# Performance work log

Hardware: AMD Instinct MI355X
Metric: run time of the kernel (lower is better)

## Reference

```python
import jax, jax.numpy as jnp
import numpy as np

N, E, IN_DIM, HID = 50000, 800000, 128, 64
NEG_SLOPE = 0.01  # torch F.leaky_relu default


def setup_inputs() -> dict:
    key = jax.random.key(0)
    ks = jax.random.split(key, 8)
    x = jax.random.normal(ks[0], (N, IN_DIM), jnp.float32)
    edge_index = jax.random.randint(ks[1], (2, E), 0, N, dtype=jnp.int32)
    edge_weight = jax.random.uniform(ks[2], (E,), jnp.float32)
    h = jnp.zeros((N, HID), jnp.float32)
    c = jnp.zeros((N, HID), jnp.float32)
    sx = 1.0 / np.sqrt(IN_DIM)
    sh = 1.0 / np.sqrt(HID)
    # gate order along leading axis: [i, f, c(tilde), o]; K=2 Chebyshev weights
    Wx = (jax.random.normal(ks[3], (4, 2, IN_DIM, HID), jnp.float32) * sx)
    bx = jnp.zeros((4, HID), jnp.float32)
    Wh = (jax.random.normal(ks[4], (4, 2, HID, HID), jnp.float32) * sh)
    bh = jnp.zeros((4, HID), jnp.float32)
    wc = jax.random.normal(ks[5], (3, HID), jnp.float32) * 0.1  # peepholes for i, f, o
    bg = jnp.zeros((4, HID), jnp.float32)
    W_head = jax.random.normal(ks[6], (HID, 1), jnp.float32) * sh
    b_head = jnp.zeros((1,), jnp.float32)
    return dict(x=x, edge_index=edge_index, edge_weight=edge_weight, h=h, c=c,
                Wx=Wx, bx=bx, Wh=Wh, bh=bh, wc=wc, bg=bg, W_head=W_head, b_head=b_head)


def _cheb_norm(src, dst, ew, n):
    # ChebConv 'sym' normalization with lambda_max=2: L_hat = -D^{-1/2} A D^{-1/2}
    # (the +1 self-loop from the Laplacian cancels against fill_value=-1)
    deg = jnp.zeros((n,), ew.dtype).at[src].add(ew)
    dinv = jnp.where(deg > 0, 1.0 / jnp.sqrt(jnp.where(deg > 0, deg, 1.0)), 0.0)
    return -dinv[src] * ew * dinv[dst]


def _prop(feat, src, dst, norm, n):
    # T1 = L_hat @ feat via edge gather + segment-sum
    return jax.ops.segment_sum(norm[:, None] * feat[src], dst, num_segments=n)


def reference(x, edge_index, edge_weight, h, c, Wx, bx, Wh, bh, wc, bg, W_head, b_head):
    n = x.shape[0]
    src, dst = edge_index[0], edge_index[1]
    norm = _cheb_norm(src, dst, edge_weight, n)
    Tx = _prop(x, src, dst, norm, n)
    Th = _prop(h, src, dst, norm, n)  # shared across all 4 h-side ChebConvs
    # z[g] = X W[g,0] + (L_hat X) W[g,1] + b  for all gates at once
    z = (jnp.einsum('nd,gdh->gnh', x, Wx[:, 0]) + jnp.einsum('nd,gdh->gnh', Tx, Wx[:, 1]) + bx[:, None, :]
         + jnp.einsum('nd,gdh->gnh', h, Wh[:, 0]) + jnp.einsum('nd,gdh->gnh', Th, Wh[:, 1]) + bh[:, None, :])
    i = jax.nn.sigmoid(z[0] + wc[0] * c + bg[0])
    f = jax.nn.sigmoid(z[1] + wc[1] * c + bg[1])
    g = jnp.tanh(z[2] + bg[2])
    c_new = f * c + i * g
    o = jax.nn.sigmoid(z[3] + wc[2] * c_new + bg[3])
    h_new = o * jnp.tanh(c_new)
    out = jax.nn.leaky_relu(h_new, NEG_SLOPE) @ W_head + b_head
    return out, h_new, c_new
```

## Files before the change

### kernel.cpp

```cpp
#include <hip/hip_runtime.h>
#include <hip/hip_bf16.h>

#define IN_DIM 128
#define HID 64
#define NEG_SLOPE 0.01f
#define CAP 5120

typedef __attribute__((ext_vector_type(8))) short short8;
typedef __attribute__((ext_vector_type(4))) short short4v;
typedef __attribute__((ext_vector_type(4))) float f32x4;
typedef unsigned short ushort_t;
typedef unsigned int uint_t;

__device__ __forceinline__ float fsig(float x) { return 1.f / (1.f + __expf(-x)); }
__device__ __forceinline__ float ftanh(float x) { return 1.f - 2.f / (__expf(2.f * x) + 1.f); }

__device__ __forceinline__ ushort_t f2bf(float f) {
    uint_t u = __float_as_uint(f);
    uint_t r = u + 0x7fffu + ((u >> 16) & 1u);
    return (ushort_t)(r >> 16);
}
__device__ __forceinline__ float bf2f(ushort_t s) { return __uint_as_float(((uint_t)s) << 16); }
__device__ __forceinline__ float bf2f_s(short s) { return bf2f((ushort_t)s); }

__global__ __launch_bounds__(256) void part_kernel(
    const int* __restrict__ src, const int* __restrict__ dst, const float* __restrict__ ew,
    const float* __restrict__ x, const float* __restrict__ h,
    const float* __restrict__ Wx, const float* __restrict__ Wh,
    int* __restrict__ cur_d, int* __restrict__ cur_s,
    int2* __restrict__ dpart, int2* __restrict__ spart,
    uint_t* __restrict__ xb_u, uint_t* __restrict__ hb_u, ushort_t* __restrict__ Wp,
    int E, int N, int nbPart) {
    __shared__ int hd[256], hs[256];
    int t = threadIdx.x;

    if ((int)blockIdx.x < nbPart) {
        hd[t] = 0; hs[t] = 0;
        __syncthreads();
        int base = blockIdx.x * 2048;
        int sv[8], dv[8]; float wv[8];
#pragma unroll
        for (int it = 0; it < 8; ++it) {
            int e = base + it * 256 + t;
            bool ok = e < E;
            sv[it] = ok ? src[e] : 0;
            dv[it] = ok ? dst[e] : 0;
            wv[it] = ok ? ew[e] : 0.f;
            if (ok) {
                atomicAdd(&hd[dv[it] >> 8], 1);
                atomicAdd(&hs[sv[it] >> 8], 1);
            }
        }
        __syncthreads();
        int nd = hd[t], ns = hs[t];
        __syncthreads();
        if (nd) hd[t] = atomicAdd(&cur_d[t * 16], nd);
        if (ns) hs[t] = atomicAdd(&cur_s[t * 16], ns);
        __syncthreads();
#pragma unroll
        for (int it = 0; it < 8; ++it) {
            int e = base + it * 256 + t;
            if (e < E) {
                int d = dv[it], s = sv[it];
                int bd = d >> 8, bs = s >> 8;
                int pd = atomicAdd(&hd[bd], 1);
                int ps = atomicAdd(&hs[bs], 1);
                dpart[(size_t)bd * CAP + pd] = make_int2(s | ((d & 255) << 16), __float_as_int(wv[it]));
                spart[(size_t)bs * CAP + ps] = make_int2(s & 255, __float_as_int(wv[it]));
            }
        }
        return;
    }

    int cb = blockIdx.x - nbPart;
    int tid = cb * 256 + t;
    int T = (gridDim.x - nbPart) * 256;
    int ncvt = N * 96;
    int nx = N * 64;
    for (int i = tid; i < ncvt; i += T) {
        if (i < nx) {
            float2 v = ((const float2*)x)[i];
            xb_u[i] = (uint_t)f2bf(v.x) | ((uint_t)f2bf(v.y) << 16);
        } else {
            int j = i - nx;
            float2 v = ((const float2*)h)[j];
            hb_u[j] = (uint_t)f2bf(v.x) | ((uint_t)f2bf(v.y) << 16);
        }
    }

    for (int idx = tid; idx < 384 * 256; idx += T) {
        int j = idx & 7;
        int tmp = idx >> 3;
        int lane = tmp & 63;
        int t2 = tmp >> 6;
        int ct = t2 & 15;
        int ks = t2 >> 4;
        int k = ks * 32 + (lane >> 4) * 8 + j;
        int colg = ct * 16 + (lane & 15);
        int g = colg >> 6, hdd = colg & 63;
        float v;
        if (k < 128)      v = Wx[((g * 2 + 0) * 128 + k) * 64 + hdd];
        else if (k < 192) v = Wh[((g * 2 + 0) * 64 + (k - 128)) * 64 + hdd];
        else if (k < 320) v = Wx[((g * 2 + 1) * 128 + (k - 192)) * 64 + hdd];
        else              v = Wh[((g * 2 + 1) * 64 + (k - 320)) * 64 + hdd];
        Wp[idx] = f2bf(v);
    }
}

__global__ __launch_bounds__(256) void deg_kernel(const int2* __restrict__ spart,
                                                  const int* __restrict__ cur_s,
                                                  float* __restrict__ dinv, int N) {
    __shared__ float df[256];
    int t = threadIdx.x, b = blockIdx.x;
    df[t] = 0.f;
    __syncthreads();
    int cnt = cur_s[b * 16];
    for (int i = t; i < cnt; i += 256) {
        int2 r = spart[(size_t)b * CAP + i];
        atomicAdd(&df[r.x & 255], __int_as_float(r.y));
    }
    __syncthreads();
    int g = b * 256 + t;
    if (g < N) {
        float dd = df[t];
        dinv[g] = dd > 0.f ? rsqrtf(dd) : 0.f;
    }
}

__global__ __launch_bounds__(256) void fillb_kernel(const int2* __restrict__ dpart,
                                                    const int* __restrict__ cur_d,
                                                    const float* __restrict__ dinv,
                                                    int* __restrict__ rowptr, int* __restrict__ rowend,
                                                    int2* __restrict__ eprm, int N) {
    __shared__ int c[256], sdata[256], pcur[256];
    __shared__ float dl[256];
    int t = threadIdx.x, b = blockIdx.x;
    c[t] = 0;
    int g = b * 256 + t;
    dl[t] = (g < N) ? dinv[g] : 0.f;
    __syncthreads();
    int cnt = cur_d[b * 16];
    for (int i = t; i < cnt; i += 256) {
        int m = dpart[(size_t)b * CAP + i].x;
        atomicAdd(&c[(m >> 16) & 255], 1);
    }
    __syncthreads();
    sdata[t] = c[t];
    __syncthreads();
    for (int off = 1; off < 256; off <<= 1) {
        int tmp = (t >= off) ? sdata[t - off] : 0;
        __syncthreads();
        sdata[t] += tmp;
        __syncthreads();
    }
    int excl = sdata[t] - c[t];
    pcur[t] = excl;
    if (g < N) {
        rowptr[g] = b * CAP + excl;
        rowend[g] = b * CAP + sdata[t];
    }
    __syncthreads();
    for (int i = t; i < cnt; i += 256) {
        int2 r = dpart[(size_t)b * CAP + i];
        int m = r.x;
        int dlo = (m >> 16) & 255;
        int s = m & 0xffff;
        float w = __int_as_float(r.y);
        int pos = atomicAdd(&pcur[dlo], 1);
        float nrm = -dinv[s] * w * dl[dlo];
        eprm[(size_t)b * CAP + pos] = make_int2(s, __float_as_int(nrm));
    }
}

#define GQ_LOAD(SS, WW, XV, HV, QOFF)                                          \
    _Pragma("unroll")                                                          \
    for (int q = 0; q < 4; ++q) {                                              \
        SS[q] = __shfl(sv, sl0 + (QOFF) + q);                                  \
        WW[q] = __shfl(wv, sl0 + (QOFF) + q);                                  \
        XV[q] = *(const short8*)(xb + (size_t)SS[q] * 128 + l16 * 8);          \
        HV[q] = *(const short4v*)(hb + (size_t)SS[q] * 64 + l16 * 4);          \
    }

#define GQ_FMA(WW, XV, HV)                                                     \
    _Pragma("unroll")                                                          \
    for (int q = 0; q < 4; ++q) {                                              \
        _Pragma("unroll")                                                      \
        for (int i = 0; i < 8; ++i) ax[i] += WW[q] * bf2f_s(XV[q][i]);         \
        _Pragma("unroll")                                                      \
        for (int i = 0; i < 4; ++i) ah[i] += WW[q] * bf2f_s(HV[q][i]);         \
    }

__global__ __launch_bounds__(256) void gather_kernel(const int* __restrict__ rowptr,
                                                     const int* __restrict__ rowend,
                                                     const int2* __restrict__ eprm,
                                                     const ushort_t* __restrict__ xb,
                                                     const ushort_t* __restrict__ hb,
                                                     ushort_t* __restrict__ Txb,
                                                     ushort_t* __restrict__ Thb, int N) {
    int lane = threadIdx.x & 63;
    int wave = threadIdx.x >> 6;
    int grp = lane >> 4, l16 = lane & 15;
    int node = blockIdx.x * 16 + wave * 4 + grp;
    bool valid = node < N;
    int p = 0, end = 0;
    if (valid) { p = rowptr[node]; end = rowend[node]; }

    float ax[8] = {0.f, 0.f, 0.f, 0.f, 0.f, 0.f, 0.f, 0.f};
    float ah[4] = {0.f, 0.f, 0.f, 0.f};

    int idx0 = p + l16;
    int2 pr = (idx0 < end) ? eprm[idx0] : make_int2(0, 0);

    int sl0 = grp * 16;
    for (int base = p; base < end; base += 16) {
        int2 cur = pr;
        int nidx = base + 16 + l16;
        if (base + 16 < end) pr = (nidx < end) ? eprm[nidx] : make_int2(0, 0);
        int sv = cur.x;
        float wv = __int_as_float(cur.y);

        int sA[4]; float wA[4]; short8 xA[4]; short4v hA[4];
        int sB[4]; float wB[4]; short8 xB[4]; short4v hB[4];
        GQ_LOAD(sA, wA, xA, hA, 0)
        GQ_LOAD(sB, wB, xB, hB, 4)
        GQ_FMA(wA, xA, hA)
        GQ_LOAD(sA, wA, xA, hA, 8)
        GQ_FMA(wB, xB, hB)
        GQ_LOAD(sB, wB, xB, hB, 12)
        GQ_FMA(wA, xA, hA)
        GQ_FMA(wB, xB, hB)
    }

    if (valid) {
        short8 tx;
#pragma unroll
        for (int i = 0; i < 8; ++i) tx[i] = (short)f2bf(ax[i]);
        *(short8*)(Txb + (size_t)node * 128 + l16 * 8) = tx;
        short4v th;
#pragma unroll
        for (int i = 0; i < 4; ++i) th[i] = (short)f2bf(ah[i]);
        *(short4v*)(Thb + (size_t)node * 64 + l16 * 4) = th;
    }
}

__global__ __launch_bounds__(256, 4) void fused_mfma(
    const ushort_t* __restrict__ xb, const ushort_t* __restrict__ hb,
    const ushort_t* __restrict__ Txb, const ushort_t* __restrict__ Thb,
    const float* __restrict__ c_in, const ushort_t* __restrict__ Wp,
    const float* __restrict__ bx, const float* __restrict__ bh,
    const float* __restrict__ wc, const float* __restrict__ bg,
    const float* __restrict__ Whead, const float* __restrict__ bhead,
    float* __restrict__ out, int N) {
    __shared__ ushort_t Bs[2][8192];
    int tid = threadIdx.x;
    int lane = tid & 63;
    int wave = tid >> 6;
    int quad = lane >> 4, m = lane & 15;
    int row0 = (blockIdx.x * 4 + wave) * 16;
    int ar = row0 + m; if (ar >= N) ar = N - 1;
    int ko = quad * 8;

    short8 afr[12];
#pragma unroll
    for (int ks = 0; ks < 12; ++ks) {
        const ushort_t* a;
        if (ks < 4)       a = xb  + (size_t)ar * 128 + ks * 32 + ko;
        else if (ks < 6)  a = hb  + (size_t)ar * 64 + (ks - 4) * 32 + ko;
        else if (ks < 10) a = Txb + (size_t)ar * 128 + (ks - 6) * 32 + ko;
        else              a = Thb + (size_t)ar * 64 + (ks - 10) * 32 + ko;
        afr[ks] = *(const short8*)a;
    }

    {
        const float4* gsrc = (const float4*)(Wp);
        float4* ldst = (float4*)Bs[0];
#pragma unroll
        for (int i = 0; i < 4; ++i) ldst[tid + 256 * i] = gsrc[tid + 256 * i];
    }

    f32x4 acc[16];
#pragma unroll
    for (int ct = 0; ct < 16; ++ct) {
        int g = ct >> 2, hd = (ct & 3) * 16 + m;
        float b = bx[g * 64 + hd] + bh[g * 64 + hd];
        f32x4 bb = {b, b, b, b};
        acc[ct] = bb;
    }

    __syncthreads();

#pragma unroll
    for (int ks = 0; ks < 12; ++ks) {
        int buf = ks & 1;
        float4 tmp[4];
        if (ks < 11) {
            const float4* gsrc = (const float4*)(Wp + (ks + 1) * 8192);
#pragma unroll
            for (int i = 0; i < 4; ++i) tmp[i] = gsrc[tid + 256 * i];
        }
        const short8* bsp = (const short8*)Bs[buf];
#pragma unroll
        for (int ct = 0; ct < 16; ++ct) {
            short8 bf = bsp[ct * 64 + lane];
            acc[ct] = __builtin_amdgcn_mfma_f32_16x16x32_bf16(afr[ks], bf, acc[ct], 0, 0, 0);
        }
        if (ks < 11) {
            float4* ldst = (float4*)Bs[buf ^ 1];
#pragma unroll
            for (int i = 0; i < 4; ++i) ldst[tid + 256 * i] = tmp[i];
            __syncthreads();
        }
    }

    float hp[4] = {0.f, 0.f, 0.f, 0.f};
    float bhv = bhead[0];

#pragma unroll
    for (int hs = 0; hs < 4; ++hs) {
        int hd = hs * 16 + m;
        float wc0 = wc[hd], wc1 = wc[64 + hd], wc2 = wc[128 + hd];
        float bg0 = bg[hd], bg1 = bg[64 + hd], bg2 = bg[128 + hd], bg3 = bg[192 + hd];
        float wh = Whead[hd];
#pragma unroll
        for (int reg = 0; reg < 4; ++reg) {
            int n = row0 + quad * 4 + reg;
            if (n < N) {
                float c_old = c_in[(size_t)n * 64 + hd];
                float zi = acc[0 * 4 + hs][reg];
                float zf = acc[1 * 4 + hs][reg];
                float zg = acc[2 * 4 + hs][reg];
                float zo = acc[3 * 4 + hs][reg];
                float ii = fsig(zi + wc0 * c_old + bg0);
                float ff = fsig(zf + wc1 * c_old + bg1);
                float gg = ftanh(zg + bg2);
                float cn = ff * c_old + ii * gg;
                float oo = fsig(zo + wc2 * cn + bg3);
                float hn = oo * ftanh(cn);
                out[N + (size_t)n * 64 + hd] = hn;
                out[N + (size_t)N * 64 + (size_t)n * 64 + hd] = cn;
                float lr = hn > 0.f ? hn : NEG_SLOPE * hn;
                hp[reg] += lr * wh;
            }
        }
    }
#pragma unroll
    for (int reg = 0; reg < 4; ++reg) {
        float v0 = hp[reg];
#pragma unroll
        for (int mask = 1; mask < 16; mask <<= 1) v0 += __shfl_xor(v0, mask);
        if (m == 0) {
            int n0_ = row0 + quad * 4 + reg;
            if (n0_ < N) out[n0_] = v0 + bhv;
        }
    }
}

extern "C" void kernel_launch(void* const* d_in, const int* in_sizes, int n_in,
                              void* d_out, int out_size, void* d_ws, size_t ws_size,
                              hipStream_t stream) {
    const float* x = (const float*)d_in[0];
    const int* ei = (const int*)d_in[1];
    const float* ew = (const float*)d_in[2];
    const float* h = (const float*)d_in[3];
    const float* c = (const float*)d_in[4];
    const float* Wx = (const float*)d_in[5];
    const float* bx = (const float*)d_in[6];
    const float* Wh = (const float*)d_in[7];
    const float* bh = (const float*)d_in[8];
    const float* wc = (const float*)d_in[9];
    const float* bg = (const float*)d_in[10];
    const float* Whead = (const float*)d_in[11];
    const float* bhead = (const float*)d_in[12];

    int N = in_sizes[0] / IN_DIM;
    int E = in_sizes[1] / 2;
    const int* src = ei;
    const int* dst = ei + E;

    int nbuck = (N + 255) >> 8;
    int nbPart = (E + 2047) / 2048;

    char* wp = (char*)d_ws;
    auto alloc = [&](size_t bytes) {
        char* p = wp;
        wp += (bytes + 255) & ~(size_t)255;
        return p;
    };
    int* cur = (int*)alloc((size_t)2 * nbuck * 16 * 4);
    int* cur_d = cur;
    int* cur_s = cur + (size_t)nbuck * 16;
    float* dinv = (float*)alloc((size_t)N * 4);
    int* rowptr = (int*)alloc((size_t)N * 4);
    int* rowend = (int*)alloc((size_t)N * 4);
    int2* dpart = (int2*)alloc((size_t)nbuck * CAP * 8);
    int2* spart = (int2*)alloc((size_t)nbuck * CAP * 8);
    int2* eprm = spart;
    ushort_t* xb = (ushort_t*)alloc((size_t)N * 128 * 2);
    ushort_t* hb = (ushort_t*)alloc((size_t)N * 64 * 2);
    ushort_t* Txb = (ushort_t*)alloc((size_t)N * 128 * 2);
    ushort_t* Thb = (ushort_t*)alloc((size_t)N * 64 * 2);
    ushort_t* Wp = (ushort_t*)alloc((size_t)384 * 256 * 2);

    hipMemsetAsync(cur, 0, (size_t)2 * nbuck * 16 * 4, stream);

    part_kernel<<<2048, 256, 0, stream>>>(src, dst, ew, x, h, Wx, Wh,
                                          cur_d, cur_s, dpart, spart,
                                          (uint_t*)xb, (uint_t*)hb, Wp, E, N, nbPart);
    deg_kernel<<<nbuck, 256, 0, stream>>>(spart, cur_s, dinv, N);
    fillb_kernel<<<nbuck, 256, 0, stream>>>(dpart, cur_d, dinv, rowptr, rowend, eprm, N);
    gather_kernel<<<(N + 15) / 16, 256, 0, stream>>>(rowptr, rowend, eprm, xb, hb, Txb, Thb, N);
    fused_mfma<<<(N + 63) / 64, 256, 0, stream>>>(xb, hb, Txb, Thb, c, Wp, bx, bh, wc, bg,
                                                  Whead, bhead, (float*)d_out, N);
}
```

Before: 240.9 us.

## Process two 16-row tiles per wave in fused MFMA kernel to reuse B fragments

Each wave now computes 32 rows instead of 16, so every weight fragment read from LDS feeds two MFMAs and the per-block weight staging into shared memory covers twice as many rows. A-fragments are now loaded inside the k-loop per step instead of all being preloaded up front. This halves the number of blocks and relaxes launch bounds to 2 blocks per CU, because the accumulators double to 128 floats per lane. The cost is higher register pressure, lower occupancy and fewer blocks for latency hiding.

```diff
diff --git a/kernel.cpp b/kernel.cpp
--- a/kernel.cpp
+++ b/kernel.cpp
@@ -243,7 +243,7 @@
     }
 }
 
-__global__ __launch_bounds__(256, 4) void fused_mfma(
+__global__ __launch_bounds__(256, 2) void fused_mfma(
     const ushort_t* __restrict__ xb, const ushort_t* __restrict__ hb,
     const ushort_t* __restrict__ Txb, const ushort_t* __restrict__ Thb,
     const float* __restrict__ c_in, const ushort_t* __restrict__ Wp,
@@ -256,20 +256,10 @@
     int lane = tid & 63;
     int wave = tid >> 6;
     int quad = lane >> 4, m = lane & 15;
-    int row0 = (blockIdx.x * 4 + wave) * 16;
-    int ar = row0 + m; if (ar >= N) ar = N - 1;
+    int rowbase = blockIdx.x * 128 + wave * 32;
     int ko = quad * 8;
-
-    short8 afr[12];
-#pragma unroll
-    for (int ks = 0; ks < 12; ++ks) {
-        const ushort_t* a;
-        if (ks < 4)       a = xb  + (size_t)ar * 128 + ks * 32 + ko;
-        else if (ks < 6)  a = hb  + (size_t)ar * 64 + (ks - 4) * 32 + ko;
-        else if (ks < 10) a = Txb + (size_t)ar * 128 + (ks - 6) * 32 + ko;
-        else              a = Thb + (size_t)ar * 64 + (ks - 10) * 32 + ko;
-        afr[ks] = *(const short8*)a;
-    }
+    int ar0 = rowbase + m;      if (ar0 >= N) ar0 = N - 1;
+    int ar1 = rowbase + 16 + m; if (ar1 >= N) ar1 = N - 1;
 
     {
         const float4* gsrc = (const float4*)(Wp);
@@ -278,13 +268,14 @@
         for (int i = 0; i < 4; ++i) ldst[tid + 256 * i] = gsrc[tid + 256 * i];
     }
 
-    f32x4 acc[16];
+    f32x4 acc[16][2];
 #pragma unroll
     for (int ct = 0; ct < 16; ++ct) {
         int g = ct >> 2, hd = (ct & 3) * 16 + m;
         float b = bx[g * 64 + hd] + bh[g * 64 + hd];
         f32x4 bb = {b, b, b, b};
-        acc[ct] = bb;
+        acc[ct][0] = bb;
+        acc[ct][1] = bb;
     }
 
     __syncthreads();
@@ -298,11 +289,23 @@
 #pragma unroll
             for (int i = 0; i < 4; ++i) tmp[i] = gsrc[tid + 256 * i];
         }
+        const ushort_t *a0, *a1;
+        if (ks < 4)       { a0 = xb  + (size_t)ar0 * 128 + ks * 32 + ko;
+                            a1 = xb  + (size_t)ar1 * 128 + ks * 32 + ko; }
+        else if (ks < 6)  { a0 = hb  + (size_t)ar0 * 64 + (ks - 4) * 32 + ko;
+                            a1 = hb  + (size_t)ar1 * 64 + (ks - 4) * 32 + ko; }
+        else if (ks < 10) { a0 = Txb + (size_t)ar0 * 128 + (ks - 6) * 32 + ko;
+                            a1 = Txb + (size_t)ar1 * 128 + (ks - 6) * 32 + ko; }
+        else              { a0 = Thb + (size_t)ar0 * 64 + (ks - 10) * 32 + ko;
+                            a1 = Thb + (size_t)ar1 * 64 + (ks - 10) * 32 + ko; }
+        short8 af0 = *(const short8*)a0;
+        short8 af1 = *(const short8*)a1;
         const short8* bsp = (const short8*)Bs[buf];
 #pragma unroll
         for (int ct = 0; ct < 16; ++ct) {
             short8 bf = bsp[ct * 64 + lane];
-            acc[ct] = __builtin_amdgcn_mfma_f32_16x16x32_bf16(afr[ks], bf, acc[ct], 0, 0, 0);
+            acc[ct][0] = __builtin_amdgcn_mfma_f32_16x16x32_bf16(af0, bf, acc[ct][0], 0, 0, 0);
+            acc[ct][1] = __builtin_amdgcn_mfma_f32_16x16x32_bf16(af1, bf, acc[ct][1], 0, 0, 0);
         }
         if (ks < 11) {
             float4* ldst = (float4*)Bs[buf ^ 1];
@@ -312,8 +315,8 @@
         }
     }
 
-    float hp[4] = {0.f, 0.f, 0.f, 0.f};
     float bhv = bhead[0];
+    float hp[2][4] = {{0.f, 0.f, 0.f, 0.f}, {0.f, 0.f, 0.f, 0.f}};
 
 #pragma unroll
     for (int hs = 0; hs < 4; ++hs) {
@@ -322,35 +325,42 @@
         float bg0 = bg[hd], bg1 = bg[64 + hd], bg2 = bg[128 + hd], bg3 = bg[192 + hd];
         float wh = Whead[hd];
 #pragma unroll
+        for (int rg = 0; rg < 2; ++rg) {
+            int row0 = rowbase + rg * 16;
+#pragma unroll
+            for (int reg = 0; reg < 4; ++reg) {
+                int n = row0 + quad * 4 + reg;
+                if (n < N) {
+                    float c_old = c_in[(size_t)n * 64 + hd];
+                    float zi = acc[0 * 4 + hs][rg][reg];
+                    float zf = acc[1 * 4 + hs][rg][reg];
+                    float zg = acc[2 * 4 + hs][rg][reg];
+                    float zo = acc[3 * 4 + hs][rg][reg];
+                    float ii = fsig(zi + wc0 * c_old + bg0);
+                    float ff = fsig(zf + wc1 * c_old + bg1);
+                    float gg = ftanh(zg + bg2);
+                    float cn = ff * c_old + ii * gg;
+                    float oo = fsig(zo + wc2 * cn + bg3);
+                    float hn = oo * ftanh(cn);
+                    out[N + (size_t)n * 64 + hd] = hn;
+                    out[N + (size_t)N * 64 + (size_t)n * 64 + hd] = cn;
+                    float lr = hn > 0.f ? hn : NEG_SLOPE * hn;
+                    hp[rg][reg] += lr * wh;
+                }
+            }
+        }
+    }
+#pragma unroll
+    for (int rg = 0; rg < 2; ++rg) {
+#pragma unroll
         for (int reg = 0; reg < 4; ++reg) {
-            int n = row0 + quad * 4 + reg;
-            if (n < N) {
-                float c_old = c_in[(size_t)n * 64 + hd];
-                float zi = acc[0 * 4 + hs][reg];
-                float zf = acc[1 * 4 + hs][reg];
-                float zg = acc[2 * 4 + hs][reg];
-                float zo = acc[3 * 4 + hs][reg];
-                float ii = fsig(zi + wc0 * c_old + bg0);
-                float ff = fsig(zf + wc1 * c_old + bg1);
-                float gg = ftanh(zg + bg2);
-                float cn = ff * c_old + ii * gg;
-                float oo = fsig(zo + wc2 * cn + bg3);
-                float hn = oo * ftanh(cn);
-                out[N + (size_t)n * 64 + hd] = hn;
-                out[N + (size_t)N * 64 + (size_t)n * 64 + hd] = cn;
-                float lr = hn > 0.f ? hn : NEG_SLOPE * hn;
-                hp[reg] += lr * wh;
+            float v0 = hp[rg][reg];
+#pragma unroll
+            for (int mask = 1; mask < 16; mask <<= 1) v0 += __shfl_xor(v0, mask);
+            if (m == 0) {
+                int n0_ = rowbase + rg * 16 + quad * 4 + reg;
+                if (n0_ < N) out[n0_] = v0 + bhv;
             }
-        }
-    }
-#pragma unroll
-    for (int reg = 0; reg < 4; ++reg) {
-        float v0 = hp[reg];
-#pragma unroll
-        for (int mask = 1; mask < 16; mask <<= 1) v0 += __shfl_xor(v0, mask);
-        if (m == 0) {
-            int n0_ = row0 + quad * 4 + reg;
-            if (n0_ < N) out[n0_] = v0 + bhv;
         }
     }
 }
@@ -409,6 +419,6 @@
     deg_kernel<<<nbuck, 256, 0, stream>>>(spart, cur_s, dinv, N);
     fillb_kernel<<<nbuck, 256, 0, stream>>>(dpart, cur_d, dinv, rowptr, rowend, eprm, N);
     gather_kernel<<<(N + 15) / 16, 256, 0, stream>>>(rowptr, rowend, eprm, xb, hb, Txb, Thb, N);
-    fused_mfma<<<(N + 63) / 64, 256, 0, stream>>>(xb, hb, Txb, Thb, c, Wp, bx, bh, wc, bg,
-                                                  Whead, bhead, (float*)d_out, N);
-}
+    fused_mfma<<<(N + 127) / 128, 256, 0, stream>>>(xb, hb, Txb, Thb, c, Wp, bx, bh, wc, bg,
+                                                    Whead, bhead, (float*)d_out, N);
+}
```

After: 241.2 us. About the same (+0.1%).
